# Kernel tuning notes

Hardware: AMD Instinct MI355X
Metric: run time of the kernel (lower is better)

Reference implementation:

```python
import jax, jax.numpy as jnp
import numpy as np

LN_EPS = 1e-5


def _layernorm(x, g, b):
    mu = x.mean(-1, keepdims=True)
    var = x.var(-1, keepdims=True)  # biased, matches torch LayerNorm
    return (x - mu) * jax.lax.rsqrt(var + LN_EPS) * g + b


def setup_inputs() -> dict:
    key = jax.random.key(0)
    ks = jax.random.split(key, 12)
    N, F, P, L, B, R, D = 100000, 128, 50000, 100, 1024, 5, 32
    return {
        "node_raw_features": jax.random.normal(ks[0], (N, F), jnp.float32),
        "retrieved_nodes": jax.random.randint(ks[1], (P, L), 0, N),
        "retrieved_indices": jax.random.randint(ks[2], (B, R), 0, P),
        "src_node_ids": jax.random.randint(ks[3], (B,), 0, N),
        "dst_node_ids": jax.random.randint(ks[4], (B,), 0, N),
        "node_interact_times": jax.random.uniform(ks[5], (B,), jnp.float32),
        "W_feat": jax.random.normal(ks[6], (F, D), jnp.float32) * 0.05,
        "b_feat": jnp.zeros((D,), jnp.float32),
        "w_struct": jax.random.normal(ks[7], (D,), jnp.float32) * 0.05,
        "b_struct": jnp.zeros((D,), jnp.float32),
        "ln_g": jnp.ones((D,), jnp.float32),
        "ln_b": jnp.zeros((D,), jnp.float32),
        "W_gcn": jax.random.normal(ks[8], (D, D), jnp.float32) * 0.05,
        "b_gcn": jnp.zeros((D,), jnp.float32),
        "W_out": jax.random.normal(ks[9], (D, D), jnp.float32) * 0.05,
        "b_out": jnp.zeros((D,), jnp.float32),
    }


def reference(node_raw_features, retrieved_nodes, retrieved_indices,
              src_node_ids, dst_node_ids, node_interact_times,
              W_feat, b_feat, w_struct, b_struct, ln_g, ln_b,
              W_gcn, b_gcn, W_out, b_out):
    # retrieval gathers
    demo_nodes = retrieved_nodes[retrieved_indices]            # [B,R,L]
    demo_raw = node_raw_features[demo_nodes]                   # [B,R,L,F]
    demo_feat = demo_raw @ W_feat + b_feat                     # [B,R,L,D]

    dst_raw = node_raw_features[dst_node_ids]                  # [B,F]
    cur_skill = dst_raw[:, 0].astype(jnp.int32)[:, None, None]
    demo_skill = demo_raw[..., 0].astype(jnp.int32)            # [B,R,L]
    sim = (demo_skill == cur_skill).astype(jnp.float32)[..., None]  # [B,R,L,1]
    fused = demo_feat + (sim * w_struct + b_struct)            # Linear(1,D) on sim

    hist = fused.mean(axis=1)                                  # [B,L,D]
    hist = _layernorm(hist, ln_g, ln_b)

    # per-sample chain graph: edge j->j+1 exists iff j+1 < num_valid
    valid = (demo_nodes[:, 0, :] > 0).sum(axis=1)              # [B]
    L = hist.shape[1]
    j = jnp.arange(L - 1)
    edge_mask = (j[None, :] + 1) < valid[:, None]              # [B,L-1]

    # GCN with self-loops: deg[v] = 1 + indegree(v)
    deg = 1.0 + jnp.pad(edge_mask.astype(hist.dtype), ((0, 0), (1, 0)))  # [B,L]
    xW = hist @ W_gcn                                          # [B,L,D]
    out = xW / deg[..., None]                                  # self-loop term 1/deg
    inv_norm = jax.lax.rsqrt(deg[:, :-1] * deg[:, 1:])         # [B,L-1]
    msg = jnp.where(edge_mask[..., None], xW[:, :-1] * inv_norm[..., None], 0.0)
    out = out + jnp.pad(msg, ((0, 0), (1, 0), (0, 0)))         # scatter to dst j+1
    gnn_out = jax.nn.relu(out + b_gcn)                         # [B,L,D]

    src_emb = gnn_out.mean(axis=1)                             # global_mean_pool
    dst_emb = dst_raw @ W_feat + b_feat

    src_emb = src_emb @ W_out + b_out
    dst_emb = dst_emb @ W_out + b_out
    # dropout is identity in eval mode
    return src_emb, dst_emb
```

## Files before the change

kernel.cpp:

```cpp
#include <hip/hip_runtime.h>

#define LN_EPS 1e-5f

static __device__ __forceinline__ float4 f4zero() { return make_float4(0.f, 0.f, 0.f, 0.f); }

__global__ __launch_bounds__(256, 8) void k_feat(
    const float* __restrict__ X, const float* __restrict__ Wf,
    const float* __restrict__ bf, float* __restrict__ feat,
    int* __restrict__ skill, int N)
{
    __shared__ float Wl[128 * 32];
    for (int i = threadIdx.x; i < 128 * 32; i += 256) Wl[i] = Wf[i];
    __syncthreads();

    const int gid = blockIdx.x * 256 + threadIdx.x;
    const int row = gid >> 3;
    const int dg  = gid & 7;
    if (row >= N) return;

    const float4* __restrict__ X4 = (const float4*)X + (size_t)row * 32;
    const float4* __restrict__ W4 = (const float4*)Wl;

    float4 acc = *(const float4*)(bf + 4 * dg);

    #pragma unroll 8
    for (int f4 = 0; f4 < 32; ++f4) {
        const float4 xv = X4[f4];
        if (f4 == 0 && dg == 0) skill[row] = (int)xv.x;
        const float4 w0 = W4[(4 * f4 + 0) * 8 + dg];
        const float4 w1 = W4[(4 * f4 + 1) * 8 + dg];
        const float4 w2 = W4[(4 * f4 + 2) * 8 + dg];
        const float4 w3 = W4[(4 * f4 + 3) * 8 + dg];
        acc.x = fmaf(xv.x, w0.x, acc.x);
        acc.y = fmaf(xv.x, w0.y, acc.y);
        acc.z = fmaf(xv.x, w0.z, acc.z);
        acc.w = fmaf(xv.x, w0.w, acc.w);
        acc.x = fmaf(xv.y, w1.x, acc.x);
        acc.y = fmaf(xv.y, w1.y, acc.y);
        acc.z = fmaf(xv.y, w1.z, acc.z);
        acc.w = fmaf(xv.y, w1.w, acc.w);
        acc.x = fmaf(xv.z, w2.x, acc.x);
        acc.y = fmaf(xv.z, w2.y, acc.y);
        acc.z = fmaf(xv.z, w2.z, acc.z);
        acc.w = fmaf(xv.z, w2.w, acc.w);
        acc.x = fmaf(xv.w, w3.x, acc.x);
        acc.y = fmaf(xv.w, w3.y, acc.y);
        acc.z = fmaf(xv.w, w3.z, acc.z);
        acc.w = fmaf(xv.w, w3.w, acc.w);
    }

    *(float4*)(feat + (size_t)row * 32 + 4 * dg) = acc;
}

__global__ __launch_bounds__(256, 8) void k_rows(
    const float* __restrict__ feat, const int* __restrict__ skill,
    const int* __restrict__ rnodes, const int* __restrict__ ridx,
    const int* __restrict__ dst_ids,
    const float* __restrict__ w_struct, const float* __restrict__ b_struct,
    const float* __restrict__ ln_g, const float* __restrict__ ln_b,
    const float* __restrict__ Wg, float* __restrict__ xw_out, int BL)
{
    __shared__ float Wgl[32 * 32];
    for (int i = threadIdx.x; i < 1024; i += 256) Wgl[i] = Wg[i];
    __syncthreads();

    const int rid = blockIdx.x * 32 + (threadIdx.x >> 3);
    if (rid >= BL) return;
    const int dg   = threadIdx.x & 7;
    const int lane = threadIdx.x & 63;
    const int b = rid / 100;
    const int l = rid - b * 100;

    const int* __restrict__ rb = ridx + b * 5;
    const int cskill = skill[dst_ids[b]];

    int nodes[5];
    #pragma unroll
    for (int r = 0; r < 5; ++r) nodes[r] = rnodes[(size_t)rb[r] * 100 + l];

    float4 acc = f4zero();
    int simc = 0;
    #pragma unroll
    for (int r = 0; r < 5; ++r) {
        simc += (skill[nodes[r]] == cskill) ? 1 : 0;
        const float4 v = *(const float4*)(feat + (size_t)nodes[r] * 32 + 4 * dg);
        acc.x += v.x; acc.y += v.y; acc.z += v.z; acc.w += v.w;
    }

    const float simf = (float)simc * 0.2f;
    {
        const float4 ws = ((const float4*)w_struct)[dg];
        const float4 bs = ((const float4*)b_struct)[dg];
        acc.x = fmaf(acc.x, 0.2f, fmaf(simf, ws.x, bs.x));
        acc.y = fmaf(acc.y, 0.2f, fmaf(simf, ws.y, bs.y));
        acc.z = fmaf(acc.z, 0.2f, fmaf(simf, ws.z, bs.z));
        acc.w = fmaf(acc.w, 0.2f, fmaf(simf, ws.w, bs.w));
    }

    float part = acc.x + acc.y + acc.z + acc.w;
    part += __shfl_xor(part, 1);
    part += __shfl_xor(part, 2);
    part += __shfl_xor(part, 4);
    const float mu = part * (1.f / 32.f);
    float dx, sq;
    dx = acc.x - mu; sq  = dx * dx;
    dx = acc.y - mu; sq  = fmaf(dx, dx, sq);
    dx = acc.z - mu; sq  = fmaf(dx, dx, sq);
    dx = acc.w - mu; sq  = fmaf(dx, dx, sq);
    sq += __shfl_xor(sq, 1);
    sq += __shfl_xor(sq, 2);
    sq += __shfl_xor(sq, 4);
    const float rs = rsqrtf(sq * (1.f / 32.f) + LN_EPS);

    float4 y;
    {
        const float4 g4 = ((const float4*)ln_g)[dg];
        const float4 b4 = ((const float4*)ln_b)[dg];
        y.x = fmaf((acc.x - mu) * rs, g4.x, b4.x);
        y.y = fmaf((acc.y - mu) * rs, g4.y, b4.y);
        y.z = fmaf((acc.z - mu) * rs, g4.z, b4.z);
        y.w = fmaf((acc.w - mu) * rs, g4.w, b4.w);
    }

    float4 o = f4zero();
    const float4* __restrict__ W4 = (const float4*)Wgl;
    const int base = lane & ~7;
    #pragma unroll
    for (int s = 0; s < 8; ++s) {
        const float hx = __shfl(y.x, base + s, 64);
        const float hy = __shfl(y.y, base + s, 64);
        const float hz = __shfl(y.z, base + s, 64);
        const float hw = __shfl(y.w, base + s, 64);
        const float4 w0 = W4[(4 * s + 0) * 8 + dg];
        const float4 w1 = W4[(4 * s + 1) * 8 + dg];
        const float4 w2 = W4[(4 * s + 2) * 8 + dg];
        const float4 w3 = W4[(4 * s + 3) * 8 + dg];
        o.x = fmaf(hx, w0.x, o.x);
        o.y = fmaf(hx, w0.y, o.y);
        o.z = fmaf(hx, w0.z, o.z);
        o.w = fmaf(hx, w0.w, o.w);
        o.x = fmaf(hy, w1.x, o.x);
        o.y = fmaf(hy, w1.y, o.y);
        o.z = fmaf(hy, w1.z, o.z);
        o.w = fmaf(hy, w1.w, o.w);
        o.x = fmaf(hz, w2.x, o.x);
        o.y = fmaf(hz, w2.y, o.y);
        o.z = fmaf(hz, w2.z, o.z);
        o.w = fmaf(hz, w2.w, o.w);
        o.x = fmaf(hw, w3.x, o.x);
        o.y = fmaf(hw, w3.y, o.y);
        o.z = fmaf(hw, w3.z, o.z);
        o.w = fmaf(hw, w3.w, o.w);
    }

    *(float4*)(xw_out + (size_t)rid * 32 + 4 * dg) = o;
}

__global__ __launch_bounds__(128) void k_tail(
    const float* __restrict__ feat, const int* __restrict__ rnodes,
    const int* __restrict__ ridx, const int* __restrict__ dst_ids,
    const float* __restrict__ xw_in, const float* __restrict__ b_gcn,
    const float* __restrict__ Wo, const float* __restrict__ b_out,
    float* __restrict__ out, int B)
{
    __shared__ float Wol[32 * 32];
    __shared__ float xwT[32][101];
    __shared__ float pooled[32];
    __shared__ int   pidx0;

    const int t = threadIdx.x, b = blockIdx.x;

    for (int i = t; i < 1024; i += 128) Wol[i] = Wo[i];
    if (t == 0) pidx0 = ridx[b * 5];
    __syncthreads();

    const int l = t;
    const int node0 = (l < 100) ? rnodes[(size_t)pidx0 * 100 + l] : 0;
    const int valid = __syncthreads_count(node0 > 0);

    float4 xw[8];
    if (l < 100) {
        const float4* xp = (const float4*)(xw_in + ((size_t)b * 100 + l) * 32);
        #pragma unroll
        for (int q = 0; q < 8; ++q) {
            xw[q] = xp[q];
            xwT[4 * q + 0][l] = xw[q].x;
            xwT[4 * q + 1][l] = xw[q].y;
            xwT[4 * q + 2][l] = xw[q].z;
            xwT[4 * q + 3][l] = xw[q].w;
        }
    }
    __syncthreads();

    if (l < 100) {
        const bool hm = (l >= 1) && (l < valid);
        const float degl  = 1.f + ((l >= 1 && l < valid) ? 1.f : 0.f);
        const float deglm = 1.f + ((l - 1 >= 1 && (l - 1) < valid) ? 1.f : 0.f);
        const float invd  = 1.f / degl;
        const float invn  = hm ? rsqrtf(deglm * degl) : 0.f;
        const int lm = hm ? (l - 1) : l;
        #define GNN_D(D, C) { \
            const float m = hm ? xwT[D][lm] * invn : 0.f; \
            const float o = fmaf(xw[(D) / 4].C, invd, m) + bg4.C; \
            xw[(D) / 4].C = fmaxf(o, 0.f); }
        #pragma unroll
        for (int q = 0; q < 8; ++q) {
            const float4 bg4 = ((const float4*)b_gcn)[q];
            GNN_D(4 * q + 0, x) GNN_D(4 * q + 1, y)
            GNN_D(4 * q + 2, z) GNN_D(4 * q + 3, w)
        }
        #undef GNN_D
    }
    __syncthreads();

    if (l < 100) {
        #pragma unroll
        for (int q = 0; q < 8; ++q) {
            xwT[4 * q + 0][l] = xw[q].x;
            xwT[4 * q + 1][l] = xw[q].y;
            xwT[4 * q + 2][l] = xw[q].z;
            xwT[4 * q + 3][l] = xw[q].w;
        }
    }
    __syncthreads();

    if (t < 32) {
        float s = 0.f;
        for (int j = 0; j < 100; ++j) s += xwT[t][j];
        pooled[t] = s * 0.01f;
    }
    __syncthreads();

    if (t < 32) {
        float s = b_out[t];
        #pragma unroll 8
        for (int k = 0; k < 32; ++k) s = fmaf(pooled[k], Wol[k * 32 + t], s);
        out[(size_t)b * 32 + t] = s;
    } else if (t < 64) {
        const int d = t - 32;
        const float* fr = feat + (size_t)dst_ids[b] * 32;
        float s = b_out[d];
        #pragma unroll 8
        for (int k = 0; k < 32; ++k) s = fmaf(fr[k], Wol[k * 32 + d], s);
        out[(size_t)B * 32 + (size_t)b * 32 + d] = s;
    }
}

extern "C" void kernel_launch(void* const* d_in, const int* in_sizes, int n_in,
                              void* d_out, int out_size, void* d_ws, size_t ws_size,
                              hipStream_t stream)
{
    const float* X      = (const float*)d_in[0];
    const int*   rnodes = (const int*)  d_in[1];
    const int*   ridx   = (const int*)  d_in[2];
    const int*   dst    = (const int*)  d_in[4];
    const float* Wf  = (const float*)d_in[6];
    const float* bf  = (const float*)d_in[7];
    const float* wst = (const float*)d_in[8];
    const float* bst = (const float*)d_in[9];
    const float* lg  = (const float*)d_in[10];
    const float* lb  = (const float*)d_in[11];
    const float* Wg  = (const float*)d_in[12];
    const float* bg  = (const float*)d_in[13];
    const float* Wo  = (const float*)d_in[14];
    const float* bo  = (const float*)d_in[15];

    const int N = in_sizes[0] / 128;
    const int B = in_sizes[4];
    const int BL = B * 100;

    float* feat  = (float*)d_ws;
    int*   skill = (int*)((char*)d_ws + (size_t)N * 32 * sizeof(float));
    size_t skill_bytes = (((size_t)N * sizeof(int)) + 15) & ~(size_t)15;
    float* xw_ws = (float*)((char*)skill + skill_bytes);
    float* out   = (float*)d_out;

    k_feat<<<(N * 8 + 255) / 256, 256, 0, stream>>>(X, Wf, bf, feat, skill, N);
    k_rows<<<(BL * 8 + 255) / 256, 256, 0, stream>>>(feat, skill, rnodes, ridx, dst,
                                                     wst, bst, lg, lb, Wg, xw_ws, BL);
    k_tail<<<B, 128, 0, stream>>>(feat, rnodes, ridx, dst, xw_ws,
                                  bg, Wo, bo, out, B);
}
```

Before: 163.3 us.

## Fuse row aggregation/LayerNorm/GCN matmul with GCN tail into one per-sample kernel

Merges the per-row gather, LayerNorm and W_gcn projection kernel with the per-sample GCN/pooling/output kernel, using one 1024-thread block per batch sample. The xW intermediate now stays in shared memory instead of going through a global workspace, which removes a kernel launch and a global write and read. The risks are large blocks with an unrealistic launch-bounds occupancy hint that may constrain registers, and lower scheduling flexibility.

```diff
diff --git a/kernel.cpp b/kernel.cpp
--- a/kernel.cpp
+++ b/kernel.cpp
@@ -52,175 +52,152 @@
     *(float4*)(feat + (size_t)row * 32 + 4 * dg) = acc;
 }
 
-__global__ __launch_bounds__(256, 8) void k_rows(
+__global__ __launch_bounds__(1024, 8) void k_fused(
     const float* __restrict__ feat, const int* __restrict__ skill,
     const int* __restrict__ rnodes, const int* __restrict__ ridx,
     const int* __restrict__ dst_ids,
     const float* __restrict__ w_struct, const float* __restrict__ b_struct,
     const float* __restrict__ ln_g, const float* __restrict__ ln_b,
-    const float* __restrict__ Wg, float* __restrict__ xw_out, int BL)
-{
-    __shared__ float Wgl[32 * 32];
-    for (int i = threadIdx.x; i < 1024; i += 256) Wgl[i] = Wg[i];
-    __syncthreads();
-
-    const int rid = blockIdx.x * 32 + (threadIdx.x >> 3);
-    if (rid >= BL) return;
-    const int dg   = threadIdx.x & 7;
-    const int lane = threadIdx.x & 63;
-    const int b = rid / 100;
-    const int l = rid - b * 100;
-
-    const int* __restrict__ rb = ridx + b * 5;
-    const int cskill = skill[dst_ids[b]];
-
-    int nodes[5];
-    #pragma unroll
-    for (int r = 0; r < 5; ++r) nodes[r] = rnodes[(size_t)rb[r] * 100 + l];
-
-    float4 acc = f4zero();
-    int simc = 0;
-    #pragma unroll
-    for (int r = 0; r < 5; ++r) {
-        simc += (skill[nodes[r]] == cskill) ? 1 : 0;
-        const float4 v = *(const float4*)(feat + (size_t)nodes[r] * 32 + 4 * dg);
-        acc.x += v.x; acc.y += v.y; acc.z += v.z; acc.w += v.w;
-    }
-
-    const float simf = (float)simc * 0.2f;
-    {
-        const float4 ws = ((const float4*)w_struct)[dg];
-        const float4 bs = ((const float4*)b_struct)[dg];
-        acc.x = fmaf(acc.x, 0.2f, fmaf(simf, ws.x, bs.x));
-        acc.y = fmaf(acc.y, 0.2f, fmaf(simf, ws.y, bs.y));
-        acc.z = fmaf(acc.z, 0.2f, fmaf(simf, ws.z, bs.z));
-        acc.w = fmaf(acc.w, 0.2f, fmaf(simf, ws.w, bs.w));
-    }
-
-    float part = acc.x + acc.y + acc.z + acc.w;
-    part += __shfl_xor(part, 1);
-    part += __shfl_xor(part, 2);
-    part += __shfl_xor(part, 4);
-    const float mu = part * (1.f / 32.f);
-    float dx, sq;
-    dx = acc.x - mu; sq  = dx * dx;
-    dx = acc.y - mu; sq  = fmaf(dx, dx, sq);
-    dx = acc.z - mu; sq  = fmaf(dx, dx, sq);
-    dx = acc.w - mu; sq  = fmaf(dx, dx, sq);
-    sq += __shfl_xor(sq, 1);
-    sq += __shfl_xor(sq, 2);
-    sq += __shfl_xor(sq, 4);
-    const float rs = rsqrtf(sq * (1.f / 32.f) + LN_EPS);
-
-    float4 y;
-    {
-        const float4 g4 = ((const float4*)ln_g)[dg];
-        const float4 b4 = ((const float4*)ln_b)[dg];
-        y.x = fmaf((acc.x - mu) * rs, g4.x, b4.x);
-        y.y = fmaf((acc.y - mu) * rs, g4.y, b4.y);
-        y.z = fmaf((acc.z - mu) * rs, g4.z, b4.z);
-        y.w = fmaf((acc.w - mu) * rs, g4.w, b4.w);
-    }
-
-    float4 o = f4zero();
-    const float4* __restrict__ W4 = (const float4*)Wgl;
-    const int base = lane & ~7;
-    #pragma unroll
-    for (int s = 0; s < 8; ++s) {
-        const float hx = __shfl(y.x, base + s, 64);
-        const float hy = __shfl(y.y, base + s, 64);
-        const float hz = __shfl(y.z, base + s, 64);
-        const float hw = __shfl(y.w, base + s, 64);
-        const float4 w0 = W4[(4 * s + 0) * 8 + dg];
-        const float4 w1 = W4[(4 * s + 1) * 8 + dg];
-        const float4 w2 = W4[(4 * s + 2) * 8 + dg];
-        const float4 w3 = W4[(4 * s + 3) * 8 + dg];
-        o.x = fmaf(hx, w0.x, o.x);
-        o.y = fmaf(hx, w0.y, o.y);
-        o.z = fmaf(hx, w0.z, o.z);
-        o.w = fmaf(hx, w0.w, o.w);
-        o.x = fmaf(hy, w1.x, o.x);
-        o.y = fmaf(hy, w1.y, o.y);
-        o.z = fmaf(hy, w1.z, o.z);
-        o.w = fmaf(hy, w1.w, o.w);
-        o.x = fmaf(hz, w2.x, o.x);
-        o.y = fmaf(hz, w2.y, o.y);
-        o.z = fmaf(hz, w2.z, o.z);
-        o.w = fmaf(hz, w2.w, o.w);
-        o.x = fmaf(hw, w3.x, o.x);
-        o.y = fmaf(hw, w3.y, o.y);
-        o.z = fmaf(hw, w3.z, o.z);
-        o.w = fmaf(hw, w3.w, o.w);
-    }
-
-    *(float4*)(xw_out + (size_t)rid * 32 + 4 * dg) = o;
-}
-
-__global__ __launch_bounds__(128) void k_tail(
-    const float* __restrict__ feat, const int* __restrict__ rnodes,
-    const int* __restrict__ ridx, const int* __restrict__ dst_ids,
-    const float* __restrict__ xw_in, const float* __restrict__ b_gcn,
+    const float* __restrict__ Wg, const float* __restrict__ b_gcn,
     const float* __restrict__ Wo, const float* __restrict__ b_out,
     float* __restrict__ out, int B)
 {
+    __shared__ float Wgl[32 * 32];
     __shared__ float Wol[32 * 32];
     __shared__ float xwT[32][101];
     __shared__ float pooled[32];
-    __shared__ int   pidx0;
 
     const int t = threadIdx.x, b = blockIdx.x;
 
-    for (int i = t; i < 1024; i += 128) Wol[i] = Wo[i];
-    if (t == 0) pidx0 = ridx[b * 5];
-    __syncthreads();
-
-    const int l = t;
-    const int node0 = (l < 100) ? rnodes[(size_t)pidx0 * 100 + l] : 0;
-    const int valid = __syncthreads_count(node0 > 0);
-
-    float4 xw[8];
-    if (l < 100) {
-        const float4* xp = (const float4*)(xw_in + ((size_t)b * 100 + l) * 32);
+    Wgl[t & 1023] = Wg[t & 1023];
+    Wol[t & 1023] = Wo[t & 1023];
+
+    const int l    = t >> 3;
+    const int dg   = t & 7;
+    const int lane = t & 63;
+    const bool act = (l < 100);
+
+    const int* __restrict__ rb = ridx + b * 5;
+    const int cskill = skill[dst_ids[b]];
+
+    int   n0 = 0;
+    int   simc = 0;
+    float4 acc = f4zero();
+
+    if (act) {
+        int nodes[5];
         #pragma unroll
-        for (int q = 0; q < 8; ++q) {
-            xw[q] = xp[q];
-            xwT[4 * q + 0][l] = xw[q].x;
-            xwT[4 * q + 1][l] = xw[q].y;
-            xwT[4 * q + 2][l] = xw[q].z;
-            xwT[4 * q + 3][l] = xw[q].w;
-        }
-    }
-    __syncthreads();
-
-    if (l < 100) {
+        for (int r = 0; r < 5; ++r) nodes[r] = rnodes[(size_t)rb[r] * 100 + l];
+        n0 = nodes[0];
+        #pragma unroll
+        for (int r = 0; r < 5; ++r) {
+            simc += (skill[nodes[r]] == cskill) ? 1 : 0;
+            const float4 v = *(const float4*)(feat + (size_t)nodes[r] * 32 + 4 * dg);
+            acc.x += v.x; acc.y += v.y; acc.z += v.z; acc.w += v.w;
+        }
+    }
+
+    const int valid = __syncthreads_count(act && dg == 0 && n0 > 0);
+
+    float4 o = f4zero();
+    if (act) {
+        const float simf = (float)simc * 0.2f;
+        {
+            const float4 ws = ((const float4*)w_struct)[dg];
+            const float4 bs = ((const float4*)b_struct)[dg];
+            acc.x = fmaf(acc.x, 0.2f, fmaf(simf, ws.x, bs.x));
+            acc.y = fmaf(acc.y, 0.2f, fmaf(simf, ws.y, bs.y));
+            acc.z = fmaf(acc.z, 0.2f, fmaf(simf, ws.z, bs.z));
+            acc.w = fmaf(acc.w, 0.2f, fmaf(simf, ws.w, bs.w));
+        }
+
+        float part = acc.x + acc.y + acc.z + acc.w;
+        part += __shfl_xor(part, 1);
+        part += __shfl_xor(part, 2);
+        part += __shfl_xor(part, 4);
+        const float mu = part * (1.f / 32.f);
+        float dx, sq;
+        dx = acc.x - mu; sq  = dx * dx;
+        dx = acc.y - mu; sq  = fmaf(dx, dx, sq);
+        dx = acc.z - mu; sq  = fmaf(dx, dx, sq);
+        dx = acc.w - mu; sq  = fmaf(dx, dx, sq);
+        sq += __shfl_xor(sq, 1);
+        sq += __shfl_xor(sq, 2);
+        sq += __shfl_xor(sq, 4);
+        const float rs = rsqrtf(sq * (1.f / 32.f) + LN_EPS);
+
+        float4 y;
+        {
+            const float4 g4 = ((const float4*)ln_g)[dg];
+            const float4 b4 = ((const float4*)ln_b)[dg];
+            y.x = fmaf((acc.x - mu) * rs, g4.x, b4.x);
+            y.y = fmaf((acc.y - mu) * rs, g4.y, b4.y);
+            y.z = fmaf((acc.z - mu) * rs, g4.z, b4.z);
+            y.w = fmaf((acc.w - mu) * rs, g4.w, b4.w);
+        }
+
+        const float4* __restrict__ W4 = (const float4*)Wgl;
+        const int base = lane & ~7;
+        #pragma unroll
+        for (int s = 0; s < 8; ++s) {
+            const float hx = __shfl(y.x, base + s, 64);
+            const float hy = __shfl(y.y, base + s, 64);
+            const float hz = __shfl(y.z, base + s, 64);
+            const float hw = __shfl(y.w, base + s, 64);
+            const float4 w0 = W4[(4 * s + 0) * 8 + dg];
+            const float4 w1 = W4[(4 * s + 1) * 8 + dg];
+            const float4 w2 = W4[(4 * s + 2) * 8 + dg];
+            const float4 w3 = W4[(4 * s + 3) * 8 + dg];
+            o.x = fmaf(hx, w0.x, o.x);
+            o.y = fmaf(hx, w0.y, o.y);
+            o.z = fmaf(hx, w0.z, o.z);
+            o.w = fmaf(hx, w0.w, o.w);
+            o.x = fmaf(hy, w1.x, o.x);
+            o.y = fmaf(hy, w1.y, o.y);
+            o.z = fmaf(hy, w1.z, o.z);
+            o.w = fmaf(hy, w1.w, o.w);
+            o.x = fmaf(hz, w2.x, o.x);
+            o.y = fmaf(hz, w2.y, o.y);
+            o.z = fmaf(hz, w2.z, o.z);
+            o.w = fmaf(hz, w2.w, o.w);
+            o.x = fmaf(hw, w3.x, o.x);
+            o.y = fmaf(hw, w3.y, o.y);
+            o.z = fmaf(hw, w3.z, o.z);
+            o.w = fmaf(hw, w3.w, o.w);
+        }
+
+        xwT[4 * dg + 0][l] = o.x;
+        xwT[4 * dg + 1][l] = o.y;
+        xwT[4 * dg + 2][l] = o.z;
+        xwT[4 * dg + 3][l] = o.w;
+    }
+    __syncthreads();
+
+    if (act) {
         const bool hm = (l >= 1) && (l < valid);
         const float degl  = 1.f + ((l >= 1 && l < valid) ? 1.f : 0.f);
         const float deglm = 1.f + ((l - 1 >= 1 && (l - 1) < valid) ? 1.f : 0.f);
         const float invd  = 1.f / degl;
         const float invn  = hm ? rsqrtf(deglm * degl) : 0.f;
         const int lm = hm ? (l - 1) : l;
-        #define GNN_D(D, C) { \
-            const float m = hm ? xwT[D][lm] * invn : 0.f; \
-            const float o = fmaf(xw[(D) / 4].C, invd, m) + bg4.C; \
-            xw[(D) / 4].C = fmaxf(o, 0.f); }
-        #pragma unroll
-        for (int q = 0; q < 8; ++q) {
-            const float4 bg4 = ((const float4*)b_gcn)[q];
-            GNN_D(4 * q + 0, x) GNN_D(4 * q + 1, y)
-            GNN_D(4 * q + 2, z) GNN_D(4 * q + 3, w)
-        }
-        #undef GNN_D
-    }
-    __syncthreads();
-
-    if (l < 100) {
-        #pragma unroll
-        for (int q = 0; q < 8; ++q) {
-            xwT[4 * q + 0][l] = xw[q].x;
-            xwT[4 * q + 1][l] = xw[q].y;
-            xwT[4 * q + 2][l] = xw[q].z;
-            xwT[4 * q + 3][l] = xw[q].w;
-        }
+        const float4 bg4 = ((const float4*)b_gcn)[dg];
+        float m;
+        m = hm ? xwT[4 * dg + 0][lm] * invn : 0.f;
+        o.x = fmaxf(fmaf(o.x, invd, m) + bg4.x, 0.f);
+        m = hm ? xwT[4 * dg + 1][lm] * invn : 0.f;
+        o.y = fmaxf(fmaf(o.y, invd, m) + bg4.y, 0.f);
+        m = hm ? xwT[4 * dg + 2][lm] * invn : 0.f;
+        o.z = fmaxf(fmaf(o.z, invd, m) + bg4.z, 0.f);
+        m = hm ? xwT[4 * dg + 3][lm] * invn : 0.f;
+        o.w = fmaxf(fmaf(o.w, invd, m) + bg4.w, 0.f);
+    }
+    __syncthreads();
+
+    if (act) {
+        xwT[4 * dg + 0][l] = o.x;
+        xwT[4 * dg + 1][l] = o.y;
+        xwT[4 * dg + 2][l] = o.z;
+        xwT[4 * dg + 3][l] = o.w;
     }
     __syncthreads();
 
@@ -267,17 +244,12 @@
 
     const int N = in_sizes[0] / 128;
     const int B = in_sizes[4];
-    const int BL = B * 100;
 
     float* feat  = (float*)d_ws;
     int*   skill = (int*)((char*)d_ws + (size_t)N * 32 * sizeof(float));
-    size_t skill_bytes = (((size_t)N * sizeof(int)) + 15) & ~(size_t)15;
-    float* xw_ws = (float*)((char*)skill + skill_bytes);
     float* out   = (float*)d_out;
 
     k_feat<<<(N * 8 + 255) / 256, 256, 0, stream>>>(X, Wf, bf, feat, skill, N);
-    k_rows<<<(BL * 8 + 255) / 256, 256, 0, stream>>>(feat, skill, rnodes, ridx, dst,
-                                                     wst, bst, lg, lb, Wg, xw_ws, BL);
-    k_tail<<<B, 128, 0, stream>>>(feat, rnodes, ridx, dst, xw_ws,
-                                  bg, Wo, bo, out, B);
+    k_fused<<<B, 1024, 0, stream>>>(feat, skill, rnodes, ridx, dst,
+                                    wst, bst, lg, lb, Wg, bg, Wo, bo, out, B);
 }
```

Result: no change. 160.6 us (-1.7%).
